# Kernel tuning notes

Hardware: AMD Instinct MI355X
Metric: run time of the kernel (lower is better)

## Reference

```python
import jax, jax.numpy as jnp
import numpy as np

HIDDEN = 1024
HEADS = 16
HEAD_DIM = HIDDEN // HEADS


def setup_inputs() -> dict:
    key = jax.random.key(0)
    ks = jax.random.split(key, 9)
    B, S, D = 8, 1370, HIDDEN
    x = jax.random.normal(ks[0], (B, S, D), dtype=jnp.float32)
    s = 1.0 / np.sqrt(D)
    Wq = jax.random.normal(ks[1], (D, D), dtype=jnp.float32) * s
    bq = jnp.zeros((D,), dtype=jnp.float32)
    Wk = jax.random.normal(ks[2], (D, D), dtype=jnp.float32) * s
    bk = jnp.zeros((D,), dtype=jnp.float32)
    Wv = jax.random.normal(ks[3], (D, D), dtype=jnp.float32) * s
    bv = jnp.zeros((D,), dtype=jnp.float32)
    Wo = jax.random.normal(ks[4], (D, D), dtype=jnp.float32) * s
    bo = jnp.zeros((D,), dtype=jnp.float32)
    return {"x": x, "Wq": Wq, "bq": bq, "Wk": Wk, "bk": bk,
            "Wv": Wv, "bv": bv, "Wo": Wo, "bo": bo}


def reference(x, Wq, bq, Wk, bk, Wv, bv, Wo, bo):
    B, S, D = x.shape
    H, Dh = HEADS, HEAD_DIM
    # separate Q/K/V projections
    q = (x @ Wq + bq).reshape(B, S, H, Dh).transpose(0, 2, 1, 3)  # [B,H,S,Dh]
    k = (x @ Wk + bk).reshape(B, S, H, Dh).transpose(0, 2, 1, 3)
    v = (x @ Wv + bv).reshape(B, S, H, Dh).transpose(0, 2, 1, 3)
    scale = jnp.asarray(Dh, q.dtype) ** -0.5
    attn = jnp.einsum('bhqd,bhkd->bhqk', q, k) * scale  # [B,H,S,S]
    attn = jax.nn.softmax(attn, axis=-1)
    out = jnp.einsum('bhqk,bhkd->bhqd', attn, v)        # [B,H,S,Dh]
    out = out.transpose(0, 2, 1, 3).reshape(B, S, D)
    return out @ Wo + bo
```

## Files before the change

kernel.cpp:

```cpp
#include <hip/hip_runtime.h>
#include <stdint.h>

#define DEV __device__ __forceinline__

typedef unsigned short u16;
typedef __attribute__((ext_vector_type(8))) __bf16 bf16x8;
typedef __attribute__((ext_vector_type(8))) u16 u16x8;
typedef __attribute__((ext_vector_type(4))) u16 u16x4;
typedef __attribute__((ext_vector_type(4))) float floatx4;

#define S_LEN 1370
#define S_PAD 1408
#define NH 16
#define DH 64
#define M_TOK (8 * S_LEN)
#define NKT (S_PAD / 64)
#define CEXP 0.18033688f

DEV u16 f2bf(float f) {
    return __builtin_bit_cast(u16, (__bf16)f);
}

typedef const __attribute__((address_space(1))) void as1_cvoid;
typedef __attribute__((address_space(3))) void as3_void;

DEV void async16(const void* g, void* s) {
    __builtin_amdgcn_global_load_lds((as1_cvoid*)g, (as3_void*)s, 16, 0, 0);
}

__global__ void cvt_bf16(const float* __restrict__ src, u16* __restrict__ dst) {
    const size_t i0 = ((size_t)blockIdx.x * 256 + threadIdx.x) * 8;
    const float4 a = *(const float4*)(src + i0);
    const float4 b = *(const float4*)(src + i0 + 4);
    u16x8 o;
    o[0] = f2bf(a.x); o[1] = f2bf(a.y); o[2] = f2bf(a.z); o[3] = f2bf(a.w);
    o[4] = f2bf(b.x); o[5] = f2bf(b.y); o[6] = f2bf(b.z); o[7] = f2bf(b.w);
    *(u16x8*)(dst + i0) = o;
}

__global__ void transpose4(const float* __restrict__ w0, const float* __restrict__ w1,
                           const float* __restrict__ w2, const float* __restrict__ w3,
                           u16* __restrict__ t0, u16* __restrict__ t1,
                           u16* __restrict__ t2, u16* __restrict__ t3) {
    __shared__ u16 tile[64][65];
    const float* src; u16* dst;
    switch (blockIdx.z) {
        case 0: src = w0; dst = t0; break;
        case 1: src = w1; dst = t1; break;
        case 2: src = w2; dst = t2; break;
        default: src = w3; dst = t3; break;
    }
    const int tx = blockIdx.x, ty = blockIdx.y, tid = threadIdx.x;
#pragma unroll
    for (int i = 0; i < 16; i++) {
        int e = i * 256 + tid, r = e >> 6, c = e & 63;
        tile[r][c] = f2bf(src[(size_t)(ty * 64 + r) * 1024 + tx * 64 + c]);
    }
    __syncthreads();
#pragma unroll
    for (int i = 0; i < 16; i++) {
        int e = i * 256 + tid, r = e >> 6, c = e & 63;
        dst[(size_t)(tx * 64 + r) * 1024 + ty * 64 + c] = tile[c][r];
    }
}

#define GEMM_KLOOP(M_, N_)                                                     \
    floatx4 acc[4][4];                                                         \
    _Pragma("unroll")                                                          \
    for (int i = 0; i < 4; i++)                                                \
        _Pragma("unroll")                                                      \
        for (int j = 0; j < 4; j++) acc[i][j] = (floatx4){0.f, 0.f, 0.f, 0.f}; \
    const int srow = tid >> 2;                                                 \
    const int kb = ((tid & 3) ^ ((tid >> 3) & 3)) * 16;     \
    const int rsw = (quad ^ ((l15 >> 1) & 3)) * 8;          \
    int ar0 = mbase + srow;          if (ar0 > (M_) - 1) ar0 = (M_) - 1;       \
    int ar1 = mbase + 64 + srow;     if (ar1 > (M_) - 1) ar1 = (M_) - 1;       \
    int br0 = nbase + srow;          if (br0 > (N_) - 1) br0 = (N_) - 1;       \
    int br1 = nbase + 64 + srow;     if (br1 > (N_) - 1) br1 = (N_) - 1;       \
    const char* pA = (const char*)A;                                           \
    const char* pB = (const char*)BT;                                          \
    char* ldsA = (char*)As + w * 1024;                                         \
    char* ldsB = (char*)Bs + w * 1024;                                         \
    for (int kt = 0; kt < 16; kt++) {                                          \
        const int koff = kt * 128 + kb;                                        \
        async16(pA + (size_t)ar0 * 2048 + koff, ldsA);                         \
        async16(pA + (size_t)ar1 * 2048 + koff, ldsA + 4096);                  \
        async16(pA + (size_t)ar0 * 2048 + koff + 64, ldsA + 8192);             \
        async16(pA + (size_t)ar1 * 2048 + koff + 64, ldsA + 8192 + 4096);      \
        async16(pB + (size_t)br0 * 2048 + koff, ldsB);                         \
        async16(pB + (size_t)br1 * 2048 + koff, ldsB + 4096);                  \
        async16(pB + (size_t)br0 * 2048 + koff + 64, ldsB + 8192);             \
        async16(pB + (size_t)br1 * 2048 + koff + 64, ldsB + 8192 + 4096);      \
        __syncthreads();                                                       \
        bf16x8 af[4][2], bfv[4][2];                                            \
        _Pragma("unroll")                                                      \
        for (int mi = 0; mi < 4; mi++) {                                       \
            af[mi][0] = __builtin_bit_cast(bf16x8,                             \
                *(const u16x8*)&As[(wm + mi * 16 + l15) * 32 + rsw]);          \
            af[mi][1] = __builtin_bit_cast(bf16x8,                             \
                *(const u16x8*)&As[4096 + (wm + mi * 16 + l15) * 32 + rsw]);   \
        }                                                                      \
        _Pragma("unroll")                                                      \
        for (int ni = 0; ni < 4; ni++) {                                       \
            bfv[ni][0] = __builtin_bit_cast(bf16x8,                            \
                *(const u16x8*)&Bs[(wn + ni * 16 + l15) * 32 + rsw]);          \
            bfv[ni][1] = __builtin_bit_cast(bf16x8,                            \
                *(const u16x8*)&Bs[4096 + (wn + ni * 16 + l15) * 32 + rsw]);   \
        }                                                                      \
        _Pragma("unroll")                                                      \
        for (int kk = 0; kk < 2; kk++)                                         \
            _Pragma("unroll")                                                  \
            for (int mi = 0; mi < 4; mi++)                                     \
                _Pragma("unroll")                                              \
                for (int ni = 0; ni < 4; ni++)                                 \
                    acc[mi][ni] = __builtin_amdgcn_mfma_f32_16x16x32_bf16(     \
                        af[mi][kk], bfv[ni][kk], acc[mi][ni], 0, 0, 0);        \
        __syncthreads();                                                       \
    }

__global__ void gemm_qkv(const u16* __restrict__ A, const u16* __restrict__ BT,
                         const float* __restrict__ bq, const float* __restrict__ bk,
                         const float* __restrict__ bv, u16* __restrict__ Cq,
                         u16* __restrict__ Ck, u16* __restrict__ VT, int M) {
    __shared__ u16 As[2 * 128 * 32];
    __shared__ u16 Bs[2 * 128 * 32];
    const int bid = blockIdx.x;
    const int xcd = bid & 7, rank = bid >> 3;
    const int mt = xcd * 11 + rank % 11;
    const int yt = rank / 11;
    if (mt >= 86) return;
    const int tid = threadIdx.x;
    const int w = tid >> 6, lane = tid & 63, quad = lane >> 4, l15 = lane & 15;
    const int mbase = mt * 128, nbase = yt * 128;
    const int wm = (w >> 1) * 64, wn = (w & 1) * 64;

    GEMM_KLOOP(M, 3072)

    const int sel = nbase >> 10;
    if (sel == 0) {
#pragma unroll
        for (int ni = 0; ni < 4; ni++) {
            const int n = nbase + wn + ni * 16 + l15;
            const float bb = bq[n];
#pragma unroll
            for (int mi = 0; mi < 4; mi++)
#pragma unroll
                for (int r = 0; r < 4; r++) {
                    const int m = mbase + wm + mi * 16 + quad * 4 + r;
                    if (m < M) Cq[(size_t)m * 1024 + n] = f2bf((acc[mi][ni][r] + bb) * CEXP);
                }
        }
    } else if (sel == 1) {
#pragma unroll
        for (int ni = 0; ni < 4; ni++) {
            const int n = nbase - 1024 + wn + ni * 16 + l15;
            const float bb = bk[n];
#pragma unroll
            for (int mi = 0; mi < 4; mi++)
#pragma unroll
                for (int r = 0; r < 4; r++) {
                    const int m = mbase + wm + mi * 16 + quad * 4 + r;
                    if (m < M) Ck[(size_t)m * 1024 + n] = f2bf(acc[mi][ni][r] + bb);
                }
        }
    } else {
#pragma unroll
        for (int ni = 0; ni < 4; ni++) {
            const int fe = nbase - 2048 + wn + ni * 16 + l15;
            const float bb = bv[fe];
            const int hh = fe >> 6, dd = fe & 63;
#pragma unroll
            for (int mi = 0; mi < 4; mi++)
#pragma unroll
                for (int r = 0; r < 4; r++) {
                    const int m = mbase + wm + mi * 16 + quad * 4 + r;
                    if (m < M) {
                        const int btk = m / S_LEN;
                        const int ss = m - btk * S_LEN;
                        VT[(size_t)((btk * NH + hh) * DH + dd) * S_PAD + ss] =
                            f2bf(acc[mi][ni][r] + bb);
                    }
                }
        }
    }
}

__global__ void gemm_o(const u16* __restrict__ A, const u16* __restrict__ BT,
                       const float* __restrict__ bias, float* __restrict__ C, int M) {
    __shared__ u16 As[2 * 128 * 32];
    __shared__ u16 Bs[2 * 128 * 32];
    const int bid = blockIdx.x;
    const int xcd = bid & 7, rank = bid >> 3;
    const int mt = xcd * 11 + rank % 11;
    const int yt = rank / 11;
    if (mt >= 86) return;
    const int tid = threadIdx.x;
    const int w = tid >> 6, lane = tid & 63, quad = lane >> 4, l15 = lane & 15;
    const int mbase = mt * 128, nbase = yt * 128;
    const int wm = (w >> 1) * 64, wn = (w & 1) * 64;

    GEMM_KLOOP(M, 1024)

#pragma unroll
    for (int ni = 0; ni < 4; ni++) {
        const int n = nbase + wn + ni * 16 + l15;
        const float bb = bias[n];
#pragma unroll
        for (int mi = 0; mi < 4; mi++)
#pragma unroll
            for (int r = 0; r < 4; r++) {
                const int m = mbase + wm + mi * 16 + quad * 4 + r;
                if (m < M) C[(size_t)m * 1024 + n] = acc[mi][ni][r] + bb;
            }
    }
}

__global__ void flash_attn(const u16* __restrict__ Q, const u16* __restrict__ K,
                           const u16* __restrict__ VT, u16* __restrict__ O) {
    __shared__ u16 Ks[2][2 * 64 * 32];
    __shared__ u16 Vs[2][2 * 64 * 32];
    __shared__ u16 Ps[4][32 * 72];

    const int tid = threadIdx.x;
    const int w = tid >> 6, lane = tid & 63, quad = lane >> 4, l15 = lane & 15;
    const int bh = blockIdx.x, b = bh >> 4, h = bh & 15;
    const int q0 = blockIdx.y * 128 + w * 32;

    bf16x8 qf[2][2];
#pragma unroll
    for (int mi = 0; mi < 2; mi++) {
        int qr = q0 + mi * 16 + l15;
        if (qr > S_LEN - 1) qr = S_LEN - 1;
        const u16* qp = Q + (size_t)(b * S_LEN + qr) * 1024 + h * 64 + quad * 8;
        qf[mi][0] = __builtin_bit_cast(bf16x8, *(const u16x8*)qp);
        qf[mi][1] = __builtin_bit_cast(bf16x8, *(const u16x8*)(qp + 32));
    }

    floatx4 o_acc[2][4];
#pragma unroll
    for (int mi = 0; mi < 2; mi++)
#pragma unroll
        for (int nd = 0; nd < 4; nd++) o_acc[mi][nd] = (floatx4){0.f, 0.f, 0.f, 0.f};
    float lacc[2] = {0.f, 0.f};

    const int lrow = lane >> 2;
    const int scol = ((lane & 3) ^ ((lane >> 3) & 3)) * 16;
    const char* Kbl = (const char*)K + ((size_t)b * S_LEN * 1024 + h * 64) * 2 + scol;
    const char* Vbl = (const char*)VT +
                      ((size_t)(bh * 64 + w * 16 + lrow) * S_PAD) * 2 + scol;
    char* KsB = (char*)Ks;
    char* VsB = (char*)Vs;
    u16* Pw = Ps[w];

    const int rcol = (quad ^ ((l15 >> 1) & 3)) * 16;

#define STAGE(KT, BI)                                                          \
    {                                                                          \
        int key_ = (KT) * 64 + w * 16 + lrow;                                  \
        if (key_ > S_LEN - 1) key_ = S_LEN - 1;                                \
        const char* kg_ = Kbl + (size_t)key_ * 2048;                           \
        char* kd_ = KsB + (BI) * 8192 + (w * 16) * 64;                         \
        async16(kg_, kd_);                                                     \
        async16(kg_ + 64, kd_ + 4096);                                         \
        const char* vg_ = Vbl + (KT) * 128;                                    \
        char* vd_ = VsB + (BI) * 8192 + (w * 16) * 64;                         \
        async16(vg_, vd_);                                                     \
        async16(vg_ + 64, vd_ + 4096);                                         \
    }

    STAGE(0, 0)
    __syncthreads();

    for (int kt = 0; kt < NKT; kt++) {
        const int bi = kt & 1;
        if (kt + 1 < NKT) STAGE(kt + 1, bi ^ 1)
        const char* KsT = KsB + bi * 8192;
        const char* VsT = VsB + bi * 8192;

        floatx4 st[2][4];
#pragma unroll
        for (int mi = 0; mi < 2; mi++)
#pragma unroll
            for (int ni = 0; ni < 4; ni++) st[mi][ni] = (floatx4){0.f, 0.f, 0.f, 0.f};
        __builtin_amdgcn_s_setprio(1);
#pragma unroll
        for (int kk = 0; kk < 2; kk++)
#pragma unroll
            for (int ni = 0; ni < 4; ni++) {
                bf16x8 kf = __builtin_bit_cast(bf16x8,
                    *(const u16x8*)(KsT + kk * 4096 + (ni * 16 + l15) * 64 + rcol));
                st[0][ni] = __builtin_amdgcn_mfma_f32_16x16x32_bf16(kf, qf[0][kk], st[0][ni], 0, 0, 0);
                st[1][ni] = __builtin_amdgcn_mfma_f32_16x16x32_bf16(kf, qf[1][kk], st[1][ni], 0, 0, 0);
            }
        __builtin_amdgcn_s_setprio(0);

        if (kt == NKT - 1) {
#pragma unroll
            for (int ni = 0; ni < 4; ni++)
#pragma unroll
                for (int r = 0; r < 4; r++) {
                    const bool oob = (kt * 64 + ni * 16 + quad * 4 + r) >= S_LEN;
                    if (oob) { st[0][ni][r] = -16384.f; st[1][ni][r] = -16384.f; }
                }
        }

#pragma unroll
        for (int mi = 0; mi < 2; mi++)
#pragma unroll
            for (int ni = 0; ni < 4; ni++) {
                u16x4 pq;
#pragma unroll
                for (int r = 0; r < 4; r++) {
                    const float p = __builtin_amdgcn_exp2f(st[mi][ni][r]);
                    lacc[mi] += p;
                    pq[r] = f2bf(p);
                }
                *(u16x4*)&Pw[(mi * 16 + l15) * 72 + ni * 16 + quad * 4] = pq;
            }

        __asm__ __volatile__("" ::: "memory");

        __builtin_amdgcn_s_setprio(1);
#pragma unroll
        for (int kk = 0; kk < 2; kk++) {
            bf16x8 pf0 = __builtin_bit_cast(bf16x8,
                *(const u16x8*)&Pw[(l15) * 72 + kk * 32 + quad * 8]);
            bf16x8 pf1 = __builtin_bit_cast(bf16x8,
                *(const u16x8*)&Pw[(16 + l15) * 72 + kk * 32 + quad * 8]);
#pragma unroll
            for (int nd = 0; nd < 4; nd++) {
                bf16x8 vf = __builtin_bit_cast(bf16x8,
                    *(const u16x8*)(VsT + kk * 4096 + (nd * 16 + l15) * 64 + rcol));
                o_acc[0][nd] = __builtin_amdgcn_mfma_f32_16x16x32_bf16(pf0, vf, o_acc[0][nd], 0, 0, 0);
                o_acc[1][nd] = __builtin_amdgcn_mfma_f32_16x16x32_bf16(pf1, vf, o_acc[1][nd], 0, 0, 0);
            }
        }
        __builtin_amdgcn_s_setprio(0);
        __syncthreads();
    }

    float linv[2];
#pragma unroll
    for (int mi = 0; mi < 2; mi++) {
        float rs = lacc[mi];
        rs += __shfl_xor(rs, 16);
        rs += __shfl_xor(rs, 32);
        linv[mi] = 1.f / rs;
    }

#pragma unroll
    for (int mi = 0; mi < 2; mi++)
#pragma unroll
        for (int r = 0; r < 4; r++) {
            const float inv = __shfl(linv[mi], quad * 4 + r);
            const int q = q0 + mi * 16 + quad * 4 + r;
            if (q < S_LEN) {
                u16* op = O + (size_t)(b * S_LEN + q) * 1024 + h * 64;
#pragma unroll
                for (int nd = 0; nd < 4; nd++)
                    op[nd * 16 + l15] = f2bf(o_acc[mi][nd][r] * inv);
            }
        }
}

extern "C" void kernel_launch(void* const* d_in, const int* in_sizes, int n_in,
                              void* d_out, int out_size, void* d_ws, size_t ws_size,
                              hipStream_t stream) {
    const float* x  = (const float*)d_in[0];
    const float* Wq = (const float*)d_in[1];
    const float* bq = (const float*)d_in[2];
    const float* Wk = (const float*)d_in[3];
    const float* bk = (const float*)d_in[4];
    const float* Wv = (const float*)d_in[5];
    const float* bv = (const float*)d_in[6];
    const float* Wo = (const float*)d_in[7];
    const float* bo = (const float*)d_in[8];
    float* out = (float*)d_out;

    u16* WqT = (u16*)d_ws;
    u16* WkT = WqT + (size_t)1024 * 1024;
    u16* WvT = WkT + (size_t)1024 * 1024;
    u16* WoT = WvT + (size_t)1024 * 1024;
    u16* xb  = WoT + (size_t)1024 * 1024;
    u16* Qb  = xb + (size_t)M_TOK * 1024;
    u16* Kb  = Qb + (size_t)M_TOK * 1024;
    u16* VTb = Kb + (size_t)M_TOK * 1024;
    u16* Ob  = VTb + (size_t)128 * 64 * S_PAD;

    cvt_bf16<<<dim3(M_TOK * 1024 / 2048), 256, 0, stream>>>(x, xb);
    transpose4<<<dim3(16, 16, 4), 256, 0, stream>>>(Wq, Wk, Wv, Wo, WqT, WkT, WvT, WoT);
    gemm_qkv<<<dim3(8 * 11 * 24), 256, 0, stream>>>(xb, WqT, bq, bk, bv, Qb, Kb, VTb, M_TOK);
    flash_attn<<<dim3(128, 11), 256, 0, stream>>>(Qb, Kb, VTb, Ob);
    gemm_o<<<dim3(8 * 11 * 8), 256, 0, stream>>>(Ob, WoT, bo, out, M_TOK);
}
```

Baseline: 345.6 us.

## Widen projection GEMM tiles to 128x256 with 512-thread blocks

Both projection GEMMs now use 128x256 output tiles computed by 8 waves (512 threads) instead of 128x128 tiles with 4 waves. Each block loads A once for twice as many output columns, which halves A-tile global and LDS traffic per output and halves the grid size. The cost is larger LDS use per block, fewer blocks in flight to spread across CUs, and a rewritten async load addressing scheme that drops the row clamp on B.

Measured after the change: 344.1 us. No clear change (-0.4%).

```diff
diff --git a/kernel.cpp b/kernel.cpp
--- a/kernel.cpp
+++ b/kernel.cpp
@@ -64,33 +64,32 @@
     }
 }
 
-#define GEMM_KLOOP(M_, N_)                                                     \
+#define GEMM_KLOOP512(M_, N_)                                                  \
     floatx4 acc[4][4];                                                         \
     _Pragma("unroll")                                                          \
     for (int i = 0; i < 4; i++)                                                \
         _Pragma("unroll")                                                      \
         for (int j = 0; j < 4; j++) acc[i][j] = (floatx4){0.f, 0.f, 0.f, 0.f}; \
-    const int srow = tid >> 2;                                                 \
-    const int kb = ((tid & 3) ^ ((tid >> 3) & 3)) * 16;     \
+    const int kb = ((lane & 3) ^ ((lane >> 3) & 3)) * 16;   \
     const int rsw = (quad ^ ((l15 >> 1) & 3)) * 8;          \
-    int ar0 = mbase + srow;          if (ar0 > (M_) - 1) ar0 = (M_) - 1;       \
-    int ar1 = mbase + 64 + srow;     if (ar1 > (M_) - 1) ar1 = (M_) - 1;       \
-    int br0 = nbase + srow;          if (br0 > (N_) - 1) br0 = (N_) - 1;       \
-    int br1 = nbase + 64 + srow;     if (br1 > (N_) - 1) br1 = (N_) - 1;       \
-    const char* pA = (const char*)A;                                           \
-    const char* pB = (const char*)BT;                                          \
-    char* ldsA = (char*)As + w * 1024;                                         \
-    char* ldsB = (char*)Bs + w * 1024;                                         \
+    int ar = mbase + w * 16 + (lane >> 2);                                     \
+    if (ar > (M_) - 1) ar = (M_) - 1;                                          \
+    const int br0 = nbase + w * 16 + (lane >> 2);             \
+    const int br1 = br0 + 128;                                \
+    const char* pa = (const char*)A + (size_t)ar * 2048 + kb;                  \
+    const char* pb0 = (const char*)BT + (size_t)br0 * 2048 + kb;               \
+    const char* pb1 = (const char*)BT + (size_t)br1 * 2048 + kb;               \
+    char* AsB = (char*)As;                                                     \
+    char* BsB = (char*)Bs;                                                     \
+    const int wb = w * 1024;                                                   \
     for (int kt = 0; kt < 16; kt++) {                                          \
-        const int koff = kt * 128 + kb;                                        \
-        async16(pA + (size_t)ar0 * 2048 + koff, ldsA);                         \
-        async16(pA + (size_t)ar1 * 2048 + koff, ldsA + 4096);                  \
-        async16(pA + (size_t)ar0 * 2048 + koff + 64, ldsA + 8192);             \
-        async16(pA + (size_t)ar1 * 2048 + koff + 64, ldsA + 8192 + 4096);      \
-        async16(pB + (size_t)br0 * 2048 + koff, ldsB);                         \
-        async16(pB + (size_t)br1 * 2048 + koff, ldsB + 4096);                  \
-        async16(pB + (size_t)br0 * 2048 + koff + 64, ldsB + 8192);             \
-        async16(pB + (size_t)br1 * 2048 + koff + 64, ldsB + 8192 + 4096);      \
+        const int koff = kt * 128;                                             \
+        async16(pa + koff, AsB + wb);                                          \
+        async16(pa + koff + 64, AsB + 8192 + wb);                              \
+        async16(pb0 + koff, BsB + wb);                                         \
+        async16(pb0 + koff + 64, BsB + 16384 + wb);                            \
+        async16(pb1 + koff, BsB + 8192 + wb);                                  \
+        async16(pb1 + koff + 64, BsB + 16384 + 8192 + wb);                     \
         __syncthreads();                                                       \
         bf16x8 af[4][2], bfv[4][2];                                            \
         _Pragma("unroll")                                                      \
@@ -105,7 +104,7 @@
             bfv[ni][0] = __builtin_bit_cast(bf16x8,                            \
                 *(const u16x8*)&Bs[(wn + ni * 16 + l15) * 32 + rsw]);          \
             bfv[ni][1] = __builtin_bit_cast(bf16x8,                            \
-                *(const u16x8*)&Bs[4096 + (wn + ni * 16 + l15) * 32 + rsw]);   \
+                *(const u16x8*)&Bs[8192 + (wn + ni * 16 + l15) * 32 + rsw]);   \
         }                                                                      \
         _Pragma("unroll")                                                      \
         for (int kk = 0; kk < 2; kk++)                                         \
@@ -118,12 +117,13 @@
         __syncthreads();                                                       \
     }
 
-__global__ void gemm_qkv(const u16* __restrict__ A, const u16* __restrict__ BT,
-                         const float* __restrict__ bq, const float* __restrict__ bk,
-                         const float* __restrict__ bv, u16* __restrict__ Cq,
-                         u16* __restrict__ Ck, u16* __restrict__ VT, int M) {
+__global__ __launch_bounds__(512) void gemm_qkv(
+        const u16* __restrict__ A, const u16* __restrict__ BT,
+        const float* __restrict__ bq, const float* __restrict__ bk,
+        const float* __restrict__ bv, u16* __restrict__ Cq,
+        u16* __restrict__ Ck, u16* __restrict__ VT, int M) {
     __shared__ u16 As[2 * 128 * 32];
-    __shared__ u16 Bs[2 * 128 * 32];
+    __shared__ u16 Bs[2 * 256 * 32];
     const int bid = blockIdx.x;
     const int xcd = bid & 7, rank = bid >> 3;
     const int mt = xcd * 11 + rank % 11;
@@ -131,10 +131,10 @@
     if (mt >= 86) return;
     const int tid = threadIdx.x;
     const int w = tid >> 6, lane = tid & 63, quad = lane >> 4, l15 = lane & 15;
-    const int mbase = mt * 128, nbase = yt * 128;
-    const int wm = (w >> 1) * 64, wn = (w & 1) * 64;
-
-    GEMM_KLOOP(M, 3072)
+    const int mbase = mt * 128, nbase = yt * 256;
+    const int wm = (w >> 2) * 64, wn = (w & 3) * 64;
+
+    GEMM_KLOOP512(M, 3072)
 
     const int sel = nbase >> 10;
     if (sel == 0) {
@@ -185,10 +185,11 @@
     }
 }
 
-__global__ void gemm_o(const u16* __restrict__ A, const u16* __restrict__ BT,
-                       const float* __restrict__ bias, float* __restrict__ C, int M) {
+__global__ __launch_bounds__(512) void gemm_o(
+        const u16* __restrict__ A, const u16* __restrict__ BT,
+        const float* __restrict__ bias, float* __restrict__ C, int M) {
     __shared__ u16 As[2 * 128 * 32];
-    __shared__ u16 Bs[2 * 128 * 32];
+    __shared__ u16 Bs[2 * 256 * 32];
     const int bid = blockIdx.x;
     const int xcd = bid & 7, rank = bid >> 3;
     const int mt = xcd * 11 + rank % 11;
@@ -196,10 +197,10 @@
     if (mt >= 86) return;
     const int tid = threadIdx.x;
     const int w = tid >> 6, lane = tid & 63, quad = lane >> 4, l15 = lane & 15;
-    const int mbase = mt * 128, nbase = yt * 128;
-    const int wm = (w >> 1) * 64, wn = (w & 1) * 64;
-
-    GEMM_KLOOP(M, 1024)
+    const int mbase = mt * 128, nbase = yt * 256;
+    const int wm = (w >> 2) * 64, wn = (w & 3) * 64;
+
+    GEMM_KLOOP512(M, 1024)
 
 #pragma unroll
     for (int ni = 0; ni < 4; ni++) {
@@ -389,7 +390,7 @@
 
     cvt_bf16<<<dim3(M_TOK * 1024 / 2048), 256, 0, stream>>>(x, xb);
     transpose4<<<dim3(16, 16, 4), 256, 0, stream>>>(Wq, Wk, Wv, Wo, WqT, WkT, WvT, WoT);
-    gemm_qkv<<<dim3(8 * 11 * 24), 256, 0, stream>>>(xb, WqT, bq, bk, bv, Qb, Kb, VTb, M_TOK);
+    gemm_qkv<<<dim3(8 * 11 * 12), 512, 0, stream>>>(xb, WqT, bq, bk, bv, Qb, Kb, VTb, M_TOK);
     flash_attn<<<dim3(128, 11), 256, 0, stream>>>(Qb, Kb, VTb, Ob);
-    gemm_o<<<dim3(8 * 11 * 8), 256, 0, stream>>>(Ob, WoT, bo, out, M_TOK);
-}
+    gemm_o<<<dim3(8 * 11 * 4), 512, 0, stream>>>(Ob, WoT, bo, out, M_TOK);
+}
```
